# Kernel tuning notes

Hardware: AMD Instinct MI355X
Metric: run time of the kernel (lower is better)

Reference implementation:

```python
import jax, jax.numpy as jnp
import numpy as np

N, E = 50000, 800000
IN = OUT = 128
T, R, H = 4, 6, 8
DK = OUT // H


def setup_inputs() -> dict:
    key = jax.random.key(0)
    ks = iter(jax.random.split(key, 24))
    nk = lambda: next(ks)
    return {
        "node_inp": jax.random.normal(nk(), (N, IN), jnp.float32),
        "node_type": jax.random.randint(nk(), (N,), 0, T),
        "edge_index": jax.random.randint(nk(), (2, E), 0, N),
        "edge_type": jax.random.randint(nk(), (E,), 0, R),
        "edge_sign": jax.random.randint(nk(), (E,), -2, 2),
        "edge_distance": jax.random.uniform(nk(), (E,), jnp.float32, 0.0, 2e5),
        "Wq": jax.random.normal(nk(), (T, IN, OUT), jnp.float32) / np.float32(np.sqrt(IN)),
        "bq": jnp.zeros((T, OUT), jnp.float32),
        "Wk": jax.random.normal(nk(), (T, IN, OUT), jnp.float32) / np.float32(np.sqrt(IN)),
        "bk": jnp.zeros((T, OUT), jnp.float32),
        "Wv": jax.random.normal(nk(), (T, IN, OUT), jnp.float32) / np.float32(np.sqrt(IN)),
        "bv": jnp.zeros((T, OUT), jnp.float32),
        "rel_q": jax.random.normal(nk(), (R, H, DK), jnp.float32) * 0.2,
        "rel_k": jax.random.normal(nk(), (R, H, DK), jnp.float32) * 0.2,
        "rel_v": jax.random.normal(nk(), (R, H, DK), jnp.float32) * 0.2,
        "sign_k_neutral": jnp.ones((H, DK), jnp.float32),
        "sign_v_neutral": jnp.ones((H, DK), jnp.float32),
        "rel_bias": jnp.zeros((R, H), jnp.float32),
        "dist_alpha": jnp.asarray(0.5, jnp.float32),
        "dist_tau": jnp.asarray(100000.0, jnp.float32),
        "skip": jnp.ones((T,), jnp.float32),
        "ln_gamma": jnp.ones((T, OUT), jnp.float32),
        "ln_beta": jnp.zeros((T, OUT), jnp.float32),
    }


def reference(node_inp, node_type, edge_index, edge_type, edge_sign, edge_distance,
              Wq, bq, Wk, bk, Wv, bv, rel_q, rel_k, rel_v,
              sign_k_neutral, sign_v_neutral, rel_bias, dist_alpha, dist_tau,
              skip, ln_gamma, ln_beta):
    n = node_inp.shape[0]
    src, dst = edge_index[0], edge_index[1]

    # edge_sign normalization: anything < -1 or == 0 -> -2 (neutral), else clamp to {-1, 1}
    es = jnp.where((edge_sign < -1) | (edge_sign == 0), -2, jnp.clip(edge_sign, -1, 1))
    sign_idx = jnp.where(es == -1, 0, jnp.where(es == 1, 1, 2))  # [E]

    # per-type Q/K/V projections, then select by node_type
    idx = jnp.arange(n)
    Q = (jnp.einsum('ni,tio->tno', node_inp, Wq) + bq[:, None, :])[node_type, idx]
    K = (jnp.einsum('ni,tio->tno', node_inp, Wk) + bk[:, None, :])[node_type, idx]
    V = (jnp.einsum('ni,tio->tno', node_inp, Wv) + bv[:, None, :])[node_type, idx]
    Q = Q.reshape(n, H, DK); K = K.reshape(n, H, DK); V = V.reshape(n, H, DK)

    sign_k_all = jnp.concatenate([-jnp.ones((1, H, DK), Q.dtype), jnp.ones((1, H, DK), Q.dtype), sign_k_neutral[None]], 0)
    sign_v_all = jnp.concatenate([-jnp.ones((1, H, DK), Q.dtype), jnp.ones((1, H, DK), Q.dtype), sign_v_neutral[None]], 0)

    q_eff = Q[dst] * rel_q[edge_type]                        # [E,H,DK]
    k_eff = K[src] * rel_k[edge_type] * sign_k_all[sign_idx]  # [E,H,DK]
    v_eff = V[src] * rel_v[edge_type] * sign_v_all[sign_idx]  # [E,H,DK]

    scores = (q_eff * k_eff).sum(-1) / np.float32(np.sqrt(DK))  # [E,H]
    scores = scores + rel_bias[edge_type]
    phi = dist_alpha * jnp.exp(-edge_distance / (dist_tau + 1e-9))
    scores = scores + phi[:, None]

    # destination-grouped softmax over edges
    m = jax.ops.segment_max(scores, dst, num_segments=n)      # [N,H]
    ex = jnp.exp(scores - m[dst])
    Z = jax.ops.segment_sum(ex, dst, num_segments=n)          # [N,H]
    attn = ex / (Z[dst] + 1e-9)                               # [E,H]

    msg = (v_eff * attn[..., None]).reshape(-1, OUT)          # [E,OUT]
    out = jax.ops.segment_sum(msg, dst, num_segments=n)       # [N,OUT]

    alpha = jax.nn.sigmoid(skip)[node_type][:, None]          # [N,1]
    mix = alpha * out + (1.0 - alpha) * node_inp
    mu = mix.mean(-1, keepdims=True)
    var = ((mix - mu) ** 2).mean(-1, keepdims=True)
    normed = (mix - mu) / jnp.sqrt(var + 1e-5)
    return normed * ln_gamma[node_type] + ln_beta[node_type]
```

## Files before the change

kernel.cpp:

```cpp
#include <hip/hip_runtime.h>

#define N_NODES 50000
#define N_EDGES 800000
#define DIM 128
#define NT 4
#define NR 6
#define NH 8
#define NBLK_SCAN ((N_NODES + 255) / 256)
#define NBLK2 ((N_NODES + 1023) / 1024)
#define NTILE_ROW 3129
#define NPAD_MAX (NTILE_ROW * 16)

#define WT_N   (NT * 3 * DIM * DIM)
#define WCB_N  (24 * 32)
#define PREP_TOTAL (WT_N + WCB_N)
#define PREP_BLOCKS ((PREP_TOTAL + 255) / 256)
#define HIST_BLOCKS (N_EDGES / 256)
#define A_PREP_BASE NBLK_SCAN
#define A_HIST_BASE (NBLK_SCAN + PREP_BLOCKS)
#define A_BLOCKS (A_HIST_BASE + HIST_BLOCKS)

#define PCHUNK 4
#define PROJ_BLOCKS ((NTILE_ROW + PCHUNK - 1) / PCHUNK)
#define EMIT_BLOCKS ((N_EDGES + 511) / 512)

typedef __attribute__((ext_vector_type(8))) short bf16x8;
typedef __attribute__((ext_vector_type(4))) float f32x4;

__device__ __forceinline__ unsigned short f2bf(float f) {
    unsigned int u = __float_as_uint(f);
    return (unsigned short)((u + 0x7fffu + ((u >> 16) & 1u)) >> 16);
}
__device__ __forceinline__ float blo(unsigned int u) { return __uint_as_float(u << 16); }
__device__ __forceinline__ float bhi(unsigned int u) { return __uint_as_float(u & 0xffff0000u); }

__device__ __forceinline__ int sign_index(int s) {
    if (s < -1 || s == 0) return 2;
    return (s == -1) ? 0 : 1;
}

__global__ __launch_bounds__(256) void k_A(
    const int* __restrict__ ntype, int* __restrict__ bhist, int* __restrict__ opad,
    const float* __restrict__ Wq, const float* __restrict__ Wk, const float* __restrict__ Wv,
    const float* __restrict__ rel_q, const float* __restrict__ rel_k,
    const float* __restrict__ rel_v,
    const float* __restrict__ skn, const float* __restrict__ svn,
    unsigned short* __restrict__ Wt, uint4* __restrict__ wcb,
    const int* __restrict__ ei, int* __restrict__ cnt, int* __restrict__ posw)
{
    int blk = blockIdx.x;
    if (blk < NBLK_SCAN) {
        __shared__ int h[NT];
        if (threadIdx.x < NT) h[threadIdx.x] = 0;
        __syncthreads();
        int n = blk * 256 + threadIdx.x;
        if (n < N_NODES) atomicAdd(&h[ntype[n]], 1);
        if (n < NPAD_MAX) opad[n] = -1;
        __syncthreads();
        if (threadIdx.x < NT) bhist[blk * NT + threadIdx.x] = h[threadIdx.x];
        return;
    }
    if (blk < A_HIST_BASE) {
        int i = (blk - A_PREP_BASE) * 256 + threadIdx.x;
        if (i < WT_N) {
            int j = i;
            int in = j & 127;
            int b2 = j >> 7;
            int out = b2 & 127;
            int ts = b2 >> 7;
            int sel = ts % 3, t = ts / 3;
            const float* W = sel == 0 ? Wq : (sel == 1 ? Wk : Wv);
            Wt[j] = f2bf(W[((size_t)t * DIM + in) * DIM + out]);
        } else if (i < PREP_TOTAL) {
            int j = i - WT_N;
            int p = j & 31;
            int cmb = j >> 5;
            int et = cmb & 7, sidx = cmb >> 3;
            if (et < NR) {
                int h2 = p >> 2;
                unsigned d[4];
                #pragma unroll
                for (int q = 0; q < 4; ++q) {
                    int o = 4 * p + q;
                    int rb = (et * NH + h2) * 16 + (o & 15);
                    float sgk = sidx == 0 ? -1.f : (sidx == 1 ? 1.f : skn[o]);
                    float sgv = sidx == 0 ? -1.f : (sidx == 1 ? 1.f : svn[o]);
                    float wk = rel_q[rb] * rel_k[rb] * sgk * 0.25f;
                    float wv = rel_v[rb] * sgv;
                    d[q] = (unsigned)f2bf(wk) | ((unsigned)f2bf(wv) << 16);
                }
                uint4 u; u.x = d[0]; u.y = d[1]; u.z = d[2]; u.w = d[3];
                wcb[cmb * 32 + p] = u;
            }
        }
        return;
    }
    int e = (blk - A_HIST_BASE) * 256 + threadIdx.x;
    if (e < N_EDGES) posw[e] = atomicAdd(&cnt[ei[N_EDGES + e]], 1);
}

__global__ __launch_bounds__(1024) void k_B(
    const int* __restrict__ bhist, int* __restrict__ bbase, int* __restrict__ pb_g,
    const int* __restrict__ cnt, int* __restrict__ offs, int* __restrict__ bsum)
{
    int tid = threadIdx.x;
    if (blockIdx.x == 0) {
        __shared__ int s[1024];
        __shared__ int pb[NT + 1];
        int t = tid / NBLK_SCAN;
        int b = tid - t * NBLK_SCAN;
        int v = (tid < NT * NBLK_SCAN) ? bhist[b * NT + t] : 0;
        s[tid] = v;
        __syncthreads();
        for (int d = 1; d < 1024; d <<= 1) {
            int add = (tid >= d) ? s[tid - d] : 0;
            __syncthreads();
            s[tid] += add;
            __syncthreads();
        }
        if (tid == 0) {
            int acc = 0;
            for (int tt = 0; tt < NT; ++tt) {
                pb[tt] = acc;
                int tot = s[(tt + 1) * NBLK_SCAN - 1] - (tt ? s[tt * NBLK_SCAN - 1] : 0);
                acc += ((tot + 15) >> 4) << 4;
            }
            pb[NT] = acc;
        }
        __syncthreads();
        if (tid < NT * NBLK_SCAN) {
            int excl = s[tid] - v;
            int base_t = t ? s[t * NBLK_SCAN - 1] : 0;
            bbase[b * NT + t] = pb[t] + (excl - base_t);
        }
        if (tid <= NT) pb_g[tid] = pb[tid];
        return;
    }
    int sb = blockIdx.x - 1;
    __shared__ int s[1024];
    int i = sb * 1024 + tid;
    int v = (i < N_NODES) ? cnt[i] : 0;
    s[tid] = v;
    __syncthreads();
    for (int d = 1; d < 1024; d <<= 1) {
        int add = (tid >= d) ? s[tid - d] : 0;
        __syncthreads();
        s[tid] += add;
        __syncthreads();
    }
    if (i < N_NODES) offs[i] = s[tid] - v;
    if (tid == 1023) bsum[sb] = s[1023];
}

__global__ __launch_bounds__(256) void k_C(
    const int* __restrict__ ntype, const int* __restrict__ bbase, int* __restrict__ order_pad,
    int* __restrict__ slot,
    const int* __restrict__ bsum, int* __restrict__ bofs, int* __restrict__ offs)
{
    int blk = blockIdx.x;
    if (blk < NBLK_SCAN) {
        __shared__ int cur[NT];
        if (threadIdx.x < NT) cur[threadIdx.x] = bbase[blk * NT + threadIdx.x];
        __syncthreads();
        int n = blk * 256 + threadIdx.x;
        if (n < N_NODES) {
            int t = ntype[n];
            int pos = atomicAdd(&cur[t], 1);
            order_pad[pos] = n;
            slot[n] = pos;
        }
        return;
    }
    __shared__ int s[256];
    int t = threadIdx.x;
    int v = (t < NBLK2) ? bsum[t] : 0;
    s[t] = v;
    __syncthreads();
    for (int d = 1; d < 256; d <<= 1) {
        int add = (t >= d) ? s[t - d] : 0;
        __syncthreads();
        s[t] += add;
        __syncthreads();
    }
    if (t < NBLK2) {
        int b = s[t] - v;
        bofs[t] = b;
        if (t == NBLK2 - 1) offs[N_NODES] = N_EDGES - b;
    }
}

__global__ __launch_bounds__(256) void k_emit(
    const int* __restrict__ slot,
    const int* __restrict__ ei, const int* __restrict__ etype,
    const int* __restrict__ esign, const float* __restrict__ edist,
    const float* __restrict__ dalpha, const float* __restrict__ dtau,
    const int* __restrict__ offs, const int* __restrict__ bofs,
    const int* __restrict__ posw, int2* __restrict__ edata)
{
    int e0 = blockIdx.x * 512 + threadIdx.x;
    if (e0 >= N_EDGES) return;
    int e1 = e0 + 256;
    bool v1 = (e1 < N_EDGES);
    int dst0 = ei[N_EDGES + e0];
    int src0 = ei[e0];
    int dst1 = v1 ? ei[N_EDGES + e1] : 0;
    int src1 = v1 ? ei[e1] : 0;
    int pw0 = posw[e0];
    int pw1 = v1 ? posw[e1] : 0;
    int sl0 = slot[src0];
    int sl1 = slot[src1];
    int of0 = offs[dst0] + bofs[dst0 >> 10];
    int of1 = offs[dst1] + bofs[dst1 >> 10];
    int cmb0 = sign_index(esign[e0]) * 8 + etype[e0];
    int cmb1 = v1 ? (sign_index(esign[e1]) * 8 + etype[e1]) : 0;
    float rtau = 1.f / (dtau[0] + 1e-9f);
    float da = dalpha[0];
    float phi0 = da * __expf(-edist[e0] * rtau);
    float phi1 = da * __expf(-(v1 ? edist[e1] : 0.f) * rtau);
    long long p0 = ((long long)(unsigned)__float_as_int(phi0) << 32)
                 | (unsigned)(sl0 | (cmb0 << 16));
    __builtin_nontemporal_store(p0, (long long*)(edata + of0 + pw0));
    if (v1) {
        long long p1 = ((long long)(unsigned)__float_as_int(phi1) << 32)
                     | (unsigned)(sl1 | (cmb1 << 16));
        __builtin_nontemporal_store(p1, (long long*)(edata + of1 + pw1));
    }
}

__global__ __launch_bounds__(256) void k_projm(
    const float* __restrict__ x, const unsigned short* __restrict__ Wt,
    const int* __restrict__ order_pad, const int* __restrict__ pb_g,
    const float* __restrict__ bq, const float* __restrict__ bk, const float* __restrict__ bv,
    float* __restrict__ Qf, unsigned int* __restrict__ KVu)
{
    const int chunk = blockIdx.x;
    const int wave = threadIdx.x >> 6, lane = threadIdx.x & 63;
    const int col = wave * 16 + (lane & 15);
    const int ko = (lane >> 4) * 8;
    const int tmax = pb_g[NT];
    const int pb1 = pb_g[1], pb2 = pb_g[2], pb3 = pb_g[3];

    bf16x8 afrag[PCHUNK][4];
    int row0s[PCHUNK];
    bool valid[PCHUNK];
    #pragma unroll
    for (int tt = 0; tt < PCHUNK; ++tt) {
        int tile = chunk * PCHUNK + tt;
        int row0 = tile * 16;
        row0s[tt] = row0;
        bool v = (tile < NTILE_ROW) && (row0 < tmax);
        valid[tt] = v;
        int arow = row0 + (lane & 15);
        int nidA = v ? order_pad[arow] : -1;
        const float* xrow = x + (size_t)(nidA < 0 ? 0 : nidA) * DIM;
        #pragma unroll
        for (int kt = 0; kt < 4; ++kt) {
            float4 a = *(const float4*)(xrow + kt * 32 + ko);
            float4 b = *(const float4*)(xrow + kt * 32 + ko + 4);
            bf16x8 f;
            f[0] = (short)f2bf(a.x); f[1] = (short)f2bf(a.y);
            f[2] = (short)f2bf(a.z); f[3] = (short)f2bf(a.w);
            f[4] = (short)f2bf(b.x); f[5] = (short)f2bf(b.y);
            f[6] = (short)f2bf(b.z); f[7] = (short)f2bf(b.w);
            afrag[tt][kt] = f;
        }
    }

    #pragma unroll
    for (int g = 0; g < 2; ++g) {
        int wcol = g * 64 + col;
        int cur_t = -1;
        bf16x8 bfr[4];
        float bias = 0.f;
        #pragma unroll
        for (int tt = 0; tt < PCHUNK; ++tt) {
            if (!valid[tt]) continue;
            int row0 = row0s[tt];
            int t = (row0 >= pb3) ? 3 : (row0 >= pb2) ? 2 : (row0 >= pb1) ? 1 : 0;
            if (t != cur_t) {
                cur_t = t;
                const unsigned short* wrow = Wt + ((size_t)(t * 3 + 0) * DIM + wcol) * DIM;
                #pragma unroll
                for (int kt = 0; kt < 4; ++kt) bfr[kt] = *(const bf16x8*)(wrow + kt * 32 + ko);
                bias = bq[t * DIM + wcol];
            }
            f32x4 acc = {0.f, 0.f, 0.f, 0.f};
            #pragma unroll
            for (int kt = 0; kt < 4; ++kt)
                acc = __builtin_amdgcn_mfma_f32_16x16x32_bf16(afrag[tt][kt], bfr[kt], acc, 0, 0, 0);
            #pragma unroll
            for (int r = 0; r < 4; ++r) {
                int lrow = (lane >> 4) * 4 + r;
                Qf[(size_t)(row0 + lrow) * DIM + wcol] = acc[r] + bias;
            }
        }
    }
    #pragma unroll
    for (int g = 0; g < 2; ++g) {
        int wcol = g * 64 + col;
        int cur_t = -1;
        bf16x8 bK[4], bV[4];
        float bk_ = 0.f, bv_ = 0.f;
        #pragma unroll
        for (int tt = 0; tt < PCHUNK; ++tt) {
            if (!valid[tt]) continue;
            int row0 = row0s[tt];
            int t = (row0 >= pb3) ? 3 : (row0 >= pb2) ? 2 : (row0 >= pb1) ? 1 : 0;
            if (t != cur_t) {
                cur_t = t;
                const unsigned short* wrowK = Wt + ((size_t)(t * 3 + 1) * DIM + wcol) * DIM;
                const unsigned short* wrowV = Wt + ((size_t)(t * 3 + 2) * DIM + wcol) * DIM;
                #pragma unroll
                for (int kt = 0; kt < 4; ++kt) {
                    bK[kt] = *(const bf16x8*)(wrowK + kt * 32 + ko);
                    bV[kt] = *(const bf16x8*)(wrowV + kt * 32 + ko);
                }
                bk_ = bk[t * DIM + wcol];
                bv_ = bv[t * DIM + wcol];
            }
            f32x4 accK = {0.f, 0.f, 0.f, 0.f};
            f32x4 accV = {0.f, 0.f, 0.f, 0.f};
            #pragma unroll
            for (int kt = 0; kt < 4; ++kt) {
                accK = __builtin_amdgcn_mfma_f32_16x16x32_bf16(afrag[tt][kt], bK[kt], accK, 0, 0, 0);
                accV = __builtin_amdgcn_mfma_f32_16x16x32_bf16(afrag[tt][kt], bV[kt], accV, 0, 0, 0);
            }
            #pragma unroll
            for (int r = 0; r < 4; ++r) {
                int lrow = (lane >> 4) * 4 + r;
                unsigned d = (unsigned)f2bf(accK[r] + bk_) | ((unsigned)f2bf(accV[r] + bv_) << 16);
                KVu[(size_t)(row0 + lrow) * DIM + wcol] = d;
            }
        }
    }
}

__global__ __launch_bounds__(256) void k_attn(
    const float4* __restrict__ Qf4, const uint4* __restrict__ KV,
    const uint4* __restrict__ WCB,
    const float* __restrict__ x, const int* __restrict__ ntype,
    const int* __restrict__ slot,
    const int* __restrict__ offs, const int* __restrict__ bofs,
    const int2* __restrict__ edata,
    const float* __restrict__ rbias, const float* __restrict__ skip,
    const float* __restrict__ gmm, const float* __restrict__ bta,
    float* __restrict__ out)
{
    __shared__ float rb_s[NR * NH];
    if (threadIdx.x < NR * NH) rb_s[threadIdx.x] = rbias[threadIdx.x];
    __syncthreads();
    const int wave = threadIdx.x >> 6, lane = threadIdx.x & 63;
    const int n = blockIdx.x * 4 + wave;
    const int p = lane & 31;
    const int hi = lane >> 5;
    const int h = p >> 2;
    const int beg = offs[n] + bofs[n >> 10];
    const int end = offs[n + 1] + bofs[(n + 1) >> 10];

    const int sl = slot[n];
    const float4 q4 = Qf4[(size_t)sl * 32 + p];

    float Z = 0.f, a0 = 0.f, a1 = 0.f, a2 = 0.f, a3 = 0.f;

    auto process = [&](int2 r) {
        int src = r.x & 0xffff;
        unsigned cmb = ((unsigned)r.x) >> 16;
        uint4 kv = KV[(size_t)src * 32 + p];
        uint4 w = WCB[cmb * 32 + p];
        float pp = (q4.x * blo(w.x)) * blo(kv.x);
        pp = fmaf(q4.y * blo(w.y), blo(kv.y), pp);
        pp = fmaf(q4.z * blo(w.z), blo(kv.z), pp);
        pp = fmaf(q4.w * blo(w.w), blo(kv.w), pp);
        pp += __shfl_xor(pp, 1, 4);
        pp += __shfl_xor(pp, 2, 4);
        float ex = __expf(pp + rb_s[(cmb & 7) * NH + h] + __int_as_float(r.y));
        Z += ex;
        a0 = fmaf(bhi(kv.x) * bhi(w.x), ex, a0);
        a1 = fmaf(bhi(kv.y) * bhi(w.y), ex, a1);
        a2 = fmaf(bhi(kv.z) * bhi(w.z), ex, a2);
        a3 = fmaf(bhi(kv.w) * bhi(w.w), ex, a3);
    };

    int rem = end - beg;
    int j = beg;
    if (rem >= 4) {
        int2 r0 = edata[j + hi];
        int2 r1 = edata[j + 2 + hi];
        while (true) {
            int2 c0 = r0, c1 = r1;
            j += 4; rem -= 4;
            if (rem >= 4) { r0 = edata[j + hi]; r1 = edata[j + 2 + hi]; }
            process(c0);
            process(c1);
            if (rem < 4) break;
        }
    }
    while (rem >= 2) {
        int2 c = edata[j + hi];
        process(c);
        j += 2; rem -= 2;
    }
    if (rem) {
        int2 r = edata[j];
        int src = r.x & 0xffff;
        unsigned cmb = ((unsigned)r.x) >> 16;
        uint4 kv = KV[(size_t)src * 32 + p];
        uint4 w = WCB[cmb * 32 + p];
        float pp = (q4.x * blo(w.x)) * blo(kv.x);
        pp = fmaf(q4.y * blo(w.y), blo(kv.y), pp);
        pp = fmaf(q4.z * blo(w.z), blo(kv.z), pp);
        pp = fmaf(q4.w * blo(w.w), blo(kv.w), pp);
        pp += __shfl_xor(pp, 1, 4);
        pp += __shfl_xor(pp, 2, 4);
        float ex = __expf(pp + rb_s[(cmb & 7) * NH + h] + __int_as_float(r.y));
        ex = hi ? 0.f : ex;
        Z += ex;
        a0 = fmaf(bhi(kv.x) * bhi(w.x), ex, a0);
        a1 = fmaf(bhi(kv.y) * bhi(w.y), ex, a1);
        a2 = fmaf(bhi(kv.z) * bhi(w.z), ex, a2);
        a3 = fmaf(bhi(kv.w) * bhi(w.w), ex, a3);
    }

    Z  += __shfl_xor(Z, 32, 64);
    a0 += __shfl_xor(a0, 32, 64);
    a1 += __shfl_xor(a1, 32, 64);
    a2 += __shfl_xor(a2, 32, 64);
    a3 += __shfl_xor(a3, 32, 64);

    float rz = 1.f / (Z + 1e-9f);
    int t = ntype[n];
    float alpha = 1.f / (1.f + __expf(-skip[t]));
    float4 x4 = ((const float4*)x)[(size_t)n * 32 + p];
    float m0 = fmaf(alpha, a0 * rz - x4.x, x4.x);
    float m1 = fmaf(alpha, a1 * rz - x4.y, x4.y);
    float m2 = fmaf(alpha, a2 * rz - x4.z, x4.z);
    float m3 = fmaf(alpha, a3 * rz - x4.w, x4.w);

    float s = (m0 + m1) + (m2 + m3);
    float s2 = fmaf(m0, m0, m1 * m1) + fmaf(m2, m2, m3 * m3);
    #pragma unroll
    for (int d = 32; d >= 1; d >>= 1) {
        s += __shfl_xor(s, d, 64);
        s2 += __shfl_xor(s2, d, 64);
    }
    float mu = s * (1.f / (2 * DIM));
    float var = s2 * (1.f / (2 * DIM)) - mu * mu;
    float rstd = rsqrtf(var + 1e-5f);
    if (hi == 0) {
        float4 g4 = ((const float4*)gmm)[t * 32 + p];
        float4 b4 = ((const float4*)bta)[t * 32 + p];
        float4 o4;
        o4.x = (m0 - mu) * rstd * g4.x + b4.x;
        o4.y = (m1 - mu) * rstd * g4.y + b4.y;
        o4.z = (m2 - mu) * rstd * g4.z + b4.z;
        o4.w = (m3 - mu) * rstd * g4.w + b4.w;
        ((float4*)out)[(size_t)n * 32 + p] = o4;
    }
}

extern "C" void kernel_launch(void* const* d_in, const int* in_sizes, int n_in,
                              void* d_out, int out_size, void* d_ws, size_t ws_size,
                              hipStream_t stream) {
    const float* x      = (const float*)d_in[0];
    const int*   ntype  = (const int*)d_in[1];
    const int*   ei     = (const int*)d_in[2];
    const int*   etype  = (const int*)d_in[3];
    const int*   esign  = (const int*)d_in[4];
    const float* edist  = (const float*)d_in[5];
    const float* Wq     = (const float*)d_in[6];
    const float* bq     = (const float*)d_in[7];
    const float* Wk     = (const float*)d_in[8];
    const float* bk     = (const float*)d_in[9];
    const float* Wv     = (const float*)d_in[10];
    const float* bv     = (const float*)d_in[11];
    const float* rel_q  = (const float*)d_in[12];
    const float* rel_k  = (const float*)d_in[13];
    const float* rel_v  = (const float*)d_in[14];
    const float* skn    = (const float*)d_in[15];
    const float* svn    = (const float*)d_in[16];
    const float* rbias  = (const float*)d_in[17];
    const float* dalpha = (const float*)d_in[18];
    const float* dtau   = (const float*)d_in[19];
    const float* skip   = (const float*)d_in[20];
    const float* gmm    = (const float*)d_in[21];
    const float* bta    = (const float*)d_in[22];
    float* out = (float*)d_out;

    char* ws = (char*)d_ws;
    float*          Qf     = (float*)         (ws + 0);
    unsigned int*   KVu    = (unsigned int*)  (ws + 25632768);
    unsigned short* Wt     = (unsigned short*)(ws + 51265536);
    uint4*          wcb    = (uint4*)         (ws + 51658752);
    int*            cnt    = (int*)           (ws + 51671040);
    int*            offs   = (int*)           (ws + 51872256);
    int*            bsum   = (int*)           (ws + 52073472);
    int*            bofs   = (int*)           (ws + 52073984);
    int*            posw   = (int*)           (ws + 52074496);
    int2*           edata  = (int2*)          (ws + 55274496);
    int*            opad   = (int*)           (ws + 61675008);
    int*            slot   = (int*)           (ws + 61875712);
    int*            bhist  = (int*)           (ws + 62076416);
    int*            bbase  = (int*)           (ws + 62080512);
    int*            pb     = (int*)           (ws + 62084608);

    hipMemsetAsync(cnt, 0, (size_t)N_NODES * 4, stream);
    k_A <<<A_BLOCKS, 256, 0, stream>>>(ntype, bhist, opad,
                                       Wq, Wk, Wv, rel_q, rel_k, rel_v, skn, svn,
                                       Wt, wcb, ei, cnt, posw);
    k_B <<<1 + NBLK2, 1024, 0, stream>>>(bhist, bbase, pb, cnt, offs, bsum);
    k_C <<<NBLK_SCAN + 1, 256, 0, stream>>>(ntype, bbase, opad, slot, bsum, bofs, offs);
    k_emit <<<EMIT_BLOCKS, 256, 0, stream>>>(slot, ei, etype, esign, edist, dalpha, dtau,
                                             offs, bofs, posw, edata);
    k_projm <<<PROJ_BLOCKS, 256, 0, stream>>>(x, Wt, opad, pb, bq, bk, bv, Qf, KVu);
    k_attn <<<N_NODES / 4, 256, 0, stream>>>((const float4*)Qf, (const uint4*)KVu,
                                             (const uint4*)wcb, x, ntype, slot, offs, bofs,
                                             edata, rbias, skip, gmm, bta, out);
}
```

Measured before the change: 180.3 us.

## Drop node-type sort; compute all four type projections and select per row

Removes the per-type histogram, scan and scatter that built a type-sorted node order and slot map. The projection kernel now works on nodes in natural order, runs the MFMA for all four types, and picks each row's result by its node type. This cuts several scan and scatter passes and the slot indirection in the edge emit and attention kernels. In exchange the projection does four times the matrix work and PCHUNK drops from 4 to 2.

```diff
diff --git a/kernel.cpp b/kernel.cpp
--- a/kernel.cpp
+++ b/kernel.cpp
@@ -6,22 +6,18 @@
 #define NT 4
 #define NR 6
 #define NH 8
-#define NBLK_SCAN ((N_NODES + 255) / 256)
 #define NBLK2 ((N_NODES + 1023) / 1024)
-#define NTILE_ROW 3129
-#define NPAD_MAX (NTILE_ROW * 16)
+#define NTILE (N_NODES / 16)
 
 #define WT_N   (NT * 3 * DIM * DIM)
 #define WCB_N  (24 * 32)
 #define PREP_TOTAL (WT_N + WCB_N)
 #define PREP_BLOCKS ((PREP_TOTAL + 255) / 256)
 #define HIST_BLOCKS (N_EDGES / 256)
-#define A_PREP_BASE NBLK_SCAN
-#define A_HIST_BASE (NBLK_SCAN + PREP_BLOCKS)
-#define A_BLOCKS (A_HIST_BASE + HIST_BLOCKS)
-
-#define PCHUNK 4
-#define PROJ_BLOCKS ((NTILE_ROW + PCHUNK - 1) / PCHUNK)
+#define A_BLOCKS (PREP_BLOCKS + HIST_BLOCKS)
+
+#define PCHUNK 2
+#define PROJ_BLOCKS ((NTILE + PCHUNK - 1) / PCHUNK)
 #define EMIT_BLOCKS ((N_EDGES + 511) / 512)
 
 typedef __attribute__((ext_vector_type(8))) short bf16x8;
@@ -40,7 +36,6 @@
 }
 
 __global__ __launch_bounds__(256) void k_A(
-    const int* __restrict__ ntype, int* __restrict__ bhist, int* __restrict__ opad,
     const float* __restrict__ Wq, const float* __restrict__ Wk, const float* __restrict__ Wv,
     const float* __restrict__ rel_q, const float* __restrict__ rel_k,
     const float* __restrict__ rel_v,
@@ -49,19 +44,8 @@
     const int* __restrict__ ei, int* __restrict__ cnt, int* __restrict__ posw)
 {
     int blk = blockIdx.x;
-    if (blk < NBLK_SCAN) {
-        __shared__ int h[NT];
-        if (threadIdx.x < NT) h[threadIdx.x] = 0;
-        __syncthreads();
-        int n = blk * 256 + threadIdx.x;
-        if (n < N_NODES) atomicAdd(&h[ntype[n]], 1);
-        if (n < NPAD_MAX) opad[n] = -1;
-        __syncthreads();
-        if (threadIdx.x < NT) bhist[blk * NT + threadIdx.x] = h[threadIdx.x];
-        return;
-    }
-    if (blk < A_HIST_BASE) {
-        int i = (blk - A_PREP_BASE) * 256 + threadIdx.x;
+    if (blk < PREP_BLOCKS) {
+        int i = blk * 256 + threadIdx.x;
         if (i < WT_N) {
             int j = i;
             int in = j & 127;
@@ -95,48 +79,15 @@
         }
         return;
     }
-    int e = (blk - A_HIST_BASE) * 256 + threadIdx.x;
+    int e = (blk - PREP_BLOCKS) * 256 + threadIdx.x;
     if (e < N_EDGES) posw[e] = atomicAdd(&cnt[ei[N_EDGES + e]], 1);
 }
 
 __global__ __launch_bounds__(1024) void k_B(
-    const int* __restrict__ bhist, int* __restrict__ bbase, int* __restrict__ pb_g,
     const int* __restrict__ cnt, int* __restrict__ offs, int* __restrict__ bsum)
 {
     int tid = threadIdx.x;
-    if (blockIdx.x == 0) {
-        __shared__ int s[1024];
-        __shared__ int pb[NT + 1];
-        int t = tid / NBLK_SCAN;
-        int b = tid - t * NBLK_SCAN;
-        int v = (tid < NT * NBLK_SCAN) ? bhist[b * NT + t] : 0;
-        s[tid] = v;
-        __syncthreads();
-        for (int d = 1; d < 1024; d <<= 1) {
-            int add = (tid >= d) ? s[tid - d] : 0;
-            __syncthreads();
-            s[tid] += add;
-            __syncthreads();
-        }
-        if (tid == 0) {
-            int acc = 0;
-            for (int tt = 0; tt < NT; ++tt) {
-                pb[tt] = acc;
-                int tot = s[(tt + 1) * NBLK_SCAN - 1] - (tt ? s[tt * NBLK_SCAN - 1] : 0);
-                acc += ((tot + 15) >> 4) << 4;
-            }
-            pb[NT] = acc;
-        }
-        __syncthreads();
-        if (tid < NT * NBLK_SCAN) {
-            int excl = s[tid] - v;
-            int base_t = t ? s[t * NBLK_SCAN - 1] : 0;
-            bbase[b * NT + t] = pb[t] + (excl - base_t);
-        }
-        if (tid <= NT) pb_g[tid] = pb[tid];
-        return;
-    }
-    int sb = blockIdx.x - 1;
+    int sb = blockIdx.x;
     __shared__ int s[1024];
     int i = sb * 1024 + tid;
     int v = (i < N_NODES) ? cnt[i] : 0;
@@ -153,24 +104,8 @@
 }
 
 __global__ __launch_bounds__(256) void k_C(
-    const int* __restrict__ ntype, const int* __restrict__ bbase, int* __restrict__ order_pad,
-    int* __restrict__ slot,
     const int* __restrict__ bsum, int* __restrict__ bofs, int* __restrict__ offs)
 {
-    int blk = blockIdx.x;
-    if (blk < NBLK_SCAN) {
-        __shared__ int cur[NT];
-        if (threadIdx.x < NT) cur[threadIdx.x] = bbase[blk * NT + threadIdx.x];
-        __syncthreads();
-        int n = blk * 256 + threadIdx.x;
-        if (n < N_NODES) {
-            int t = ntype[n];
-            int pos = atomicAdd(&cur[t], 1);
-            order_pad[pos] = n;
-            slot[n] = pos;
-        }
-        return;
-    }
     __shared__ int s[256];
     int t = threadIdx.x;
     int v = (t < NBLK2) ? bsum[t] : 0;
@@ -190,7 +125,6 @@
 }
 
 __global__ __launch_bounds__(256) void k_emit(
-    const int* __restrict__ slot,
     const int* __restrict__ ei, const int* __restrict__ etype,
     const int* __restrict__ esign, const float* __restrict__ edist,
     const float* __restrict__ dalpha, const float* __restrict__ dtau,
@@ -207,8 +141,6 @@
     int src1 = v1 ? ei[e1] : 0;
     int pw0 = posw[e0];
     int pw1 = v1 ? posw[e1] : 0;
-    int sl0 = slot[src0];
-    int sl1 = slot[src1];
     int of0 = offs[dst0] + bofs[dst0 >> 10];
     int of1 = offs[dst1] + bofs[dst1 >> 10];
     int cmb0 = sign_index(esign[e0]) * 8 + etype[e0];
@@ -218,18 +150,18 @@
     float phi0 = da * __expf(-edist[e0] * rtau);
     float phi1 = da * __expf(-(v1 ? edist[e1] : 0.f) * rtau);
     long long p0 = ((long long)(unsigned)__float_as_int(phi0) << 32)
-                 | (unsigned)(sl0 | (cmb0 << 16));
+                 | (unsigned)(src0 | (cmb0 << 16));
     __builtin_nontemporal_store(p0, (long long*)(edata + of0 + pw0));
     if (v1) {
         long long p1 = ((long long)(unsigned)__float_as_int(phi1) << 32)
-                     | (unsigned)(sl1 | (cmb1 << 16));
+                     | (unsigned)(src1 | (cmb1 << 16));
         __builtin_nontemporal_store(p1, (long long*)(edata + of1 + pw1));
     }
 }
 
 __global__ __launch_bounds__(256) void k_projm(
     const float* __restrict__ x, const unsigned short* __restrict__ Wt,
-    const int* __restrict__ order_pad, const int* __restrict__ pb_g,
+    const int* __restrict__ ntype,
     const float* __restrict__ bq, const float* __restrict__ bk, const float* __restrict__ bv,
     float* __restrict__ Qf, unsigned int* __restrict__ KVu)
 {
@@ -237,10 +169,9 @@
     const int wave = threadIdx.x >> 6, lane = threadIdx.x & 63;
     const int col = wave * 16 + (lane & 15);
     const int ko = (lane >> 4) * 8;
-    const int tmax = pb_g[NT];
-    const int pb1 = pb_g[1], pb2 = pb_g[2], pb3 = pb_g[3];
 
     bf16x8 afrag[PCHUNK][4];
+    int nt_[PCHUNK][4];
     int row0s[PCHUNK];
     bool valid[PCHUNK];
     #pragma unroll
@@ -248,11 +179,9 @@
         int tile = chunk * PCHUNK + tt;
         int row0 = tile * 16;
         row0s[tt] = row0;
-        bool v = (tile < NTILE_ROW) && (row0 < tmax);
+        bool v = (tile < NTILE);
         valid[tt] = v;
-        int arow = row0 + (lane & 15);
-        int nidA = v ? order_pad[arow] : -1;
-        const float* xrow = x + (size_t)(nidA < 0 ? 0 : nidA) * DIM;
+        const float* xrow = x + (size_t)(v ? row0 + (lane & 15) : 0) * DIM;
         #pragma unroll
         for (int kt = 0; kt < 4; ++kt) {
             float4 a = *(const float4*)(xrow + kt * 32 + ko);
@@ -264,72 +193,89 @@
             f[6] = (short)f2bf(b.z); f[7] = (short)f2bf(b.w);
             afrag[tt][kt] = f;
         }
+        int base = v ? row0 + (lane >> 4) * 4 : 0;
+        int4 nt4 = *(const int4*)(ntype + base);
+        nt_[tt][0] = nt4.x; nt_[tt][1] = nt4.y; nt_[tt][2] = nt4.z; nt_[tt][3] = nt4.w;
     }
 
     #pragma unroll
     for (int g = 0; g < 2; ++g) {
         int wcol = g * 64 + col;
-        int cur_t = -1;
-        bf16x8 bfr[4];
-        float bias = 0.f;
+        float outq[PCHUNK][4];
+        #pragma unroll
+        for (int tt = 0; tt < PCHUNK; ++tt)
+            outq[tt][0] = outq[tt][1] = outq[tt][2] = outq[tt][3] = 0.f;
+        #pragma unroll
+        for (int t = 0; t < NT; ++t) {
+            const unsigned short* wrow = Wt + ((size_t)(t * 3 + 0) * DIM + wcol) * DIM;
+            bf16x8 bfr[4];
+            #pragma unroll
+            for (int kt = 0; kt < 4; ++kt) bfr[kt] = *(const bf16x8*)(wrow + kt * 32 + ko);
+            float bias = bq[t * DIM + wcol];
+            #pragma unroll
+            for (int tt = 0; tt < PCHUNK; ++tt) {
+                if (!valid[tt]) continue;
+                f32x4 acc = {0.f, 0.f, 0.f, 0.f};
+                #pragma unroll
+                for (int kt = 0; kt < 4; ++kt)
+                    acc = __builtin_amdgcn_mfma_f32_16x16x32_bf16(afrag[tt][kt], bfr[kt], acc, 0, 0, 0);
+                #pragma unroll
+                for (int r = 0; r < 4; ++r)
+                    if (nt_[tt][r] == t) outq[tt][r] = acc[r] + bias;
+            }
+        }
         #pragma unroll
         for (int tt = 0; tt < PCHUNK; ++tt) {
             if (!valid[tt]) continue;
-            int row0 = row0s[tt];
-            int t = (row0 >= pb3) ? 3 : (row0 >= pb2) ? 2 : (row0 >= pb1) ? 1 : 0;
-            if (t != cur_t) {
-                cur_t = t;
-                const unsigned short* wrow = Wt + ((size_t)(t * 3 + 0) * DIM + wcol) * DIM;
-                #pragma unroll
-                for (int kt = 0; kt < 4; ++kt) bfr[kt] = *(const bf16x8*)(wrow + kt * 32 + ko);
-                bias = bq[t * DIM + wcol];
-            }
-            f32x4 acc = {0.f, 0.f, 0.f, 0.f};
-            #pragma unroll
-            for (int kt = 0; kt < 4; ++kt)
-                acc = __builtin_amdgcn_mfma_f32_16x16x32_bf16(afrag[tt][kt], bfr[kt], acc, 0, 0, 0);
             #pragma unroll
             for (int r = 0; r < 4; ++r) {
                 int lrow = (lane >> 4) * 4 + r;
-                Qf[(size_t)(row0 + lrow) * DIM + wcol] = acc[r] + bias;
+                Qf[(size_t)(row0s[tt] + lrow) * DIM + wcol] = outq[tt][r];
             }
         }
     }
     #pragma unroll
     for (int g = 0; g < 2; ++g) {
         int wcol = g * 64 + col;
-        int cur_t = -1;
-        bf16x8 bK[4], bV[4];
-        float bk_ = 0.f, bv_ = 0.f;
+        float outK[PCHUNK][4], outV[PCHUNK][4];
+        #pragma unroll
+        for (int tt = 0; tt < PCHUNK; ++tt)
+            #pragma unroll
+            for (int r = 0; r < 4; ++r) { outK[tt][r] = 0.f; outV[tt][r] = 0.f; }
+        #pragma unroll
+        for (int t = 0; t < NT; ++t) {
+            const unsigned short* wrowK = Wt + ((size_t)(t * 3 + 1) * DIM + wcol) * DIM;
+            const unsigned short* wrowV = Wt + ((size_t)(t * 3 + 2) * DIM + wcol) * DIM;
+            bf16x8 bK[4], bV[4];
+            #pragma unroll
+            for (int kt = 0; kt < 4; ++kt) {
+                bK[kt] = *(const bf16x8*)(wrowK + kt * 32 + ko);
+                bV[kt] = *(const bf16x8*)(wrowV + kt * 32 + ko);
+            }
+            float bk_ = bk[t * DIM + wcol], bv_ = bv[t * DIM + wcol];
+            #pragma unroll
+            for (int tt = 0; tt < PCHUNK; ++tt) {
+                if (!valid[tt]) continue;
+                f32x4 accK = {0.f, 0.f, 0.f, 0.f};
+                f32x4 accV = {0.f, 0.f, 0.f, 0.f};
+                #pragma unroll
+                for (int kt = 0; kt < 4; ++kt) {
+                    accK = __builtin_amdgcn_mfma_f32_16x16x32_bf16(afrag[tt][kt], bK[kt], accK, 0, 0, 0);
+                    accV = __builtin_amdgcn_mfma_f32_16x16x32_bf16(afrag[tt][kt], bV[kt], accV, 0, 0, 0);
+                }
+                #pragma unroll
+                for (int r = 0; r < 4; ++r)
+                    if (nt_[tt][r] == t) { outK[tt][r] = accK[r] + bk_; outV[tt][r] = accV[r] + bv_; }
+            }
+        }
         #pragma unroll
         for (int tt = 0; tt < PCHUNK; ++tt) {
             if (!valid[tt]) continue;
-            int row0 = row0s[tt];
-            int t = (row0 >= pb3) ? 3 : (row0 >= pb2) ? 2 : (row0 >= pb1) ? 1 : 0;
-            if (t != cur_t) {
-                cur_t = t;
-                const unsigned short* wrowK = Wt + ((size_t)(t * 3 + 1) * DIM + wcol) * DIM;
-                const unsigned short* wrowV = Wt + ((size_t)(t * 3 + 2) * DIM + wcol) * DIM;
-                #pragma unroll
-                for (int kt = 0; kt < 4; ++kt) {
-                    bK[kt] = *(const bf16x8*)(wrowK + kt * 32 + ko);
-                    bV[kt] = *(const bf16x8*)(wrowV + kt * 32 + ko);
-                }
-                bk_ = bk[t * DIM + wcol];
-                bv_ = bv[t * DIM + wcol];
-            }
-            f32x4 accK = {0.f, 0.f, 0.f, 0.f};
-            f32x4 accV = {0.f, 0.f, 0.f, 0.f};
-            #pragma unroll
-            for (int kt = 0; kt < 4; ++kt) {
-                accK = __builtin_amdgcn_mfma_f32_16x16x32_bf16(afrag[tt][kt], bK[kt], accK, 0, 0, 0);
-                accV = __builtin_amdgcn_mfma_f32_16x16x32_bf16(afrag[tt][kt], bV[kt], accV, 0, 0, 0);
-            }
             #pragma unroll
             for (int r = 0; r < 4; ++r) {
                 int lrow = (lane >> 4) * 4 + r;
-                unsigned d = (unsigned)f2bf(accK[r] + bk_) | ((unsigned)f2bf(accV[r] + bv_) << 16);
-                KVu[(size_t)(row0 + lrow) * DIM + wcol] = d;
+                unsigned d = (unsigned)f2bf(outK[tt][r]) | ((unsigned)f2bf(outV[tt][r]) << 16);
+                KVu[(size_t)(row0s[tt] + lrow) * DIM + wcol] = d;
             }
         }
     }
@@ -339,7 +285,6 @@
     const float4* __restrict__ Qf4, const uint4* __restrict__ KV,
     const uint4* __restrict__ WCB,
     const float* __restrict__ x, const int* __restrict__ ntype,
-    const int* __restrict__ slot,
     const int* __restrict__ offs, const int* __restrict__ bofs,
     const int2* __restrict__ edata,
     const float* __restrict__ rbias, const float* __restrict__ skip,
@@ -357,8 +302,7 @@
     const int beg = offs[n] + bofs[n >> 10];
     const int end = offs[n + 1] + bofs[(n + 1) >> 10];
 
-    const int sl = slot[n];
-    const float4 q4 = Qf4[(size_t)sl * 32 + p];
+    const float4 q4 = Qf4[(size_t)n * 32 + p];
 
     float Z = 0.f, a0 = 0.f, a1 = 0.f, a2 = 0.f, a3 = 0.f;
 
@@ -488,31 +432,25 @@
 
     char* ws = (char*)d_ws;
     float*          Qf     = (float*)         (ws + 0);
-    unsigned int*   KVu    = (unsigned int*)  (ws + 25632768);
-    unsigned short* Wt     = (unsigned short*)(ws + 51265536);
-    uint4*          wcb    = (uint4*)         (ws + 51658752);
-    int*            cnt    = (int*)           (ws + 51671040);
-    int*            offs   = (int*)           (ws + 51872256);
-    int*            bsum   = (int*)           (ws + 52073472);
-    int*            bofs   = (int*)           (ws + 52073984);
-    int*            posw   = (int*)           (ws + 52074496);
-    int2*           edata  = (int2*)          (ws + 55274496);
-    int*            opad   = (int*)           (ws + 61675008);
-    int*            slot   = (int*)           (ws + 61875712);
-    int*            bhist  = (int*)           (ws + 62076416);
-    int*            bbase  = (int*)           (ws + 62080512);
-    int*            pb     = (int*)           (ws + 62084608);
+    unsigned int*   KVu    = (unsigned int*)  (ws + 25600000);
+    unsigned short* Wt     = (unsigned short*)(ws + 51200000);
+    uint4*          wcb    = (uint4*)         (ws + 51593216);
+    int*            cnt    = (int*)           (ws + 51605504);
+    int*            offs   = (int*)           (ws + 51805696);
+    int*            bsum   = (int*)           (ws + 52006400);
+    int*            bofs   = (int*)           (ws + 52006912);
+    int*            posw   = (int*)           (ws + 52007424);
+    int2*           edata  = (int2*)          (ws + 55207424);
 
     hipMemsetAsync(cnt, 0, (size_t)N_NODES * 4, stream);
-    k_A <<<A_BLOCKS, 256, 0, stream>>>(ntype, bhist, opad,
-                                       Wq, Wk, Wv, rel_q, rel_k, rel_v, skn, svn,
+    k_A <<<A_BLOCKS, 256, 0, stream>>>(Wq, Wk, Wv, rel_q, rel_k, rel_v, skn, svn,
                                        Wt, wcb, ei, cnt, posw);
-    k_B <<<1 + NBLK2, 1024, 0, stream>>>(bhist, bbase, pb, cnt, offs, bsum);
-    k_C <<<NBLK_SCAN + 1, 256, 0, stream>>>(ntype, bbase, opad, slot, bsum, bofs, offs);
-    k_emit <<<EMIT_BLOCKS, 256, 0, stream>>>(slot, ei, etype, esign, edist, dalpha, dtau,
+    k_B <<<NBLK2, 1024, 0, stream>>>(cnt, offs, bsum);
+    k_C <<<1, 256, 0, stream>>>(bsum, bofs, offs);
+    k_emit <<<EMIT_BLOCKS, 256, 0, stream>>>(ei, etype, esign, edist, dalpha, dtau,
                                              offs, bofs, posw, edata);
-    k_projm <<<PROJ_BLOCKS, 256, 0, stream>>>(x, Wt, opad, pb, bq, bk, bv, Qf, KVu);
+    k_projm <<<PROJ_BLOCKS, 256, 0, stream>>>(x, Wt, ntype, bq, bk, bv, Qf, KVu);
     k_attn <<<N_NODES / 4, 256, 0, stream>>>((const float4*)Qf, (const uint4*)KVu,
-                                             (const uint4*)wcb, x, ntype, slot, offs, bofs,
+                                             (const uint4*)wcb, x, ntype, offs, bofs,
                                              edata, rbias, skip, gmm, bta, out);
 }
```

Measured after the change: 234.3 us. +29.9%, slower.
